# Kernel tuning notes

Hardware: AMD Instinct MI355X
Metric: run time of the kernel (lower is better)

The kernel has to match this reference:

```python
import jax, jax.numpy as jnp
import numpy as np

DIM = 1024
N_EXPERTS = 8
TOP_K = 2
EXPERT_HIDDEN = DIM * 2
B, T = 4, 4096


def setup_inputs() -> dict:
    key = jax.random.key(0)
    ks = jax.random.split(key, 5)
    # xavier_uniform with gain=0.02 for w1/w2 (fan_in=DIM, fan_out=EXPERT_HIDDEN)
    lim12 = 0.02 * np.sqrt(6.0 / (DIM + EXPERT_HIDDEN))
    lim3 = 0.02 * np.sqrt(6.0 / (EXPERT_HIDDEN + DIM))
    x = jax.random.normal(ks[0], (B, T, DIM), dtype=jnp.float32)
    router_w = 0.02 * jax.random.normal(ks[1], (N_EXPERTS, DIM), dtype=jnp.float32)
    w1 = jax.random.uniform(ks[2], (N_EXPERTS, DIM, EXPERT_HIDDEN), minval=-lim12, maxval=lim12, dtype=jnp.float32)
    w2 = jax.random.uniform(ks[3], (N_EXPERTS, DIM, EXPERT_HIDDEN), minval=-lim12, maxval=lim12, dtype=jnp.float32)
    w3 = jax.random.uniform(ks[4], (N_EXPERTS, EXPERT_HIDDEN, DIM), minval=-lim3, maxval=lim3, dtype=jnp.float32)
    return {"x": x, "router_w": router_w, "w1": w1, "w2": w2, "w3": w3}


def reference(x, router_w, w1, w2, w3):
    # Router: top-k softmax gating, renormalized over the selected k.
    logits = jnp.einsum('btd,ed->bte', x, router_w)          # [B,T,E]
    probs = jax.nn.softmax(logits, axis=-1)
    topk_vals, topk_idx = jax.lax.top_k(probs, TOP_K)        # [B,T,K]
    topk_weights = topk_vals / topk_vals.sum(axis=-1, keepdims=True)

    out = jnp.zeros_like(x)
    for e in range(N_EXPERTS):
        # gate weight for expert e per token (0 if e not in token's top-k)
        w_e = jnp.where(topk_idx == e, topk_weights, 0.0).sum(axis=-1)  # [B,T]
        h = jax.nn.silu(jnp.einsum('btd,dh->bth', x, w1[e])) * jnp.einsum('btd,dh->bth', x, w2[e])
        out = out + jnp.einsum('bth,hd->btd', h, w3[e]) * w_e[..., None]
    aux_loss = jnp.float32(0.0)  # eval mode
    return (out, aux_loss)
```

## Files before the change

### kernel.cpp

```cpp
#include <hip/hip_runtime.h>
#include <stdint.h>

#define TTOK 16384
#define NDIM 1024
#define NHID 2048
#define NEXP 8
#define TM 256
#define MAXT 136
#define SLOTCAP (2 * TTOK + NEXP * TM)

typedef __attribute__((ext_vector_type(8))) short short8;
typedef __attribute__((ext_vector_type(4))) float f32x4;

__device__ __forceinline__ unsigned short f2bf(float f) {
  unsigned int u = __float_as_uint(f);
  u += 0x7FFFu + ((u >> 16) & 1u);
  return (unsigned short)(u >> 16);
}

__device__ __forceinline__ void gload16(const void* g, void* l) {
  __builtin_amdgcn_global_load_lds(
      (const __attribute__((address_space(1))) unsigned int*)g,
      (__attribute__((address_space(3))) unsigned int*)l, 16, 0, 0);
}

__device__ __forceinline__ float silu(float z) {
  return z / (1.0f + __expf(-z));
}

__device__ __forceinline__ void router_block(int b, const float* __restrict__ x,
                                             const float* __restrict__ rw,
                                             unsigned short* __restrict__ xbf,
                                             int* __restrict__ tok_e,
                                             float* __restrict__ tok_gw) {
  int t = (b << 2) + (threadIdx.x >> 6);
  int lane = threadIdx.x & 63;
  const float4* xr = (const float4*)(x + (size_t)t * NDIM);

  float4 v[4];
  float d[NEXP];
#pragma unroll
  for (int e = 0; e < NEXP; ++e) d[e] = 0.f;

#pragma unroll
  for (int i = 0; i < 4; ++i) {
    int c = i * 64 + lane;
    v[i] = xr[c];
#pragma unroll
    for (int e = 0; e < NEXP; ++e) {
      float4 w = ((const float4*)(rw + e * NDIM))[c];
      d[e] += v[i].x * w.x + v[i].y * w.y + v[i].z * w.z + v[i].w * w.w;
    }
  }
#pragma unroll
  for (int e = 0; e < NEXP; ++e)
    for (int s = 32; s; s >>= 1) d[e] += __shfl_xor(d[e], s, 64);

  unsigned short* xo = xbf + (size_t)t * NDIM;
#pragma unroll
  for (int i = 0; i < 4; ++i) {
    int c = i * 64 + lane;
    ushort4 u;
    u.x = f2bf(v[i].x); u.y = f2bf(v[i].y); u.z = f2bf(v[i].z); u.w = f2bf(v[i].w);
    ((ushort4*)xo)[c] = u;
  }

  if (lane == 0) {
    float m = d[0];
#pragma unroll
    for (int e = 1; e < NEXP; ++e) m = fmaxf(m, d[e]);
    float ex[NEXP];
#pragma unroll
    for (int e = 0; e < NEXP; ++e) ex[e] = __expf(d[e] - m);
    int e0 = 0;
#pragma unroll
    for (int e = 1; e < NEXP; ++e) if (ex[e] > ex[e0]) e0 = e;
    int e1 = (e0 == 0) ? 1 : 0;
#pragma unroll
    for (int e = 0; e < NEXP; ++e) if (e != e0 && ex[e] > ex[e1]) e1 = e;
    float p0 = ex[e0], p1 = ex[e1];
    float inv = 1.f / (p0 + p1);
    tok_e[2 * t] = e0; tok_e[2 * t + 1] = e1;
    tok_gw[2 * t] = p0 * inv; tok_gw[2 * t + 1] = p1 * inv;
  }
}

__device__ __forceinline__ void tconv_tile(const float* __restrict__ src,
                                           unsigned short* __restrict__ dst,
                                           int R, int C, int bx, int by) {
  __shared__ unsigned short tile[64][65];
  int tx = threadIdx.x & 15, ty = threadIdx.x >> 4;
#pragma unroll
  for (int rr = 0; rr < 4; ++rr) {
    int rl = rr * 16 + ty;
    float4 v = *(const float4*)(src + (size_t)(by + rl) * C + bx + tx * 4);
    tile[rl][tx * 4 + 0] = f2bf(v.x);
    tile[rl][tx * 4 + 1] = f2bf(v.y);
    tile[rl][tx * 4 + 2] = f2bf(v.z);
    tile[rl][tx * 4 + 3] = f2bf(v.w);
  }
  __syncthreads();
#pragma unroll
  for (int rr = 0; rr < 4; ++rr) {
    int cl = rr * 16 + ty;
    ushort4 u;
    u.x = tile[tx * 4 + 0][cl];
    u.y = tile[tx * 4 + 1][cl];
    u.z = tile[tx * 4 + 2][cl];
    u.w = tile[tx * 4 + 3][cl];
    *(ushort4*)(dst + (size_t)(bx + cl) * R + by + tx * 4) = u;
  }
}

__global__ void k_prep(const float* __restrict__ x, const float* __restrict__ rw,
                       unsigned short* __restrict__ xbf, int* __restrict__ tok_e,
                       float* __restrict__ tok_gw, const float* __restrict__ w1,
                       const float* __restrict__ w2, const float* __restrict__ w3,
                       unsigned short* __restrict__ w1t, unsigned short* __restrict__ w2t,
                       unsigned short* __restrict__ w3t) {
  int b = blockIdx.x;
  if (b < 4096) {
    router_block(b, x, rw, xbf, tok_e, tok_gw);
    return;
  }
  int tcb = b - 4096;
  int bx = tcb & 31;
  int by = (tcb >> 5) & 15;
  int z = tcb >> 9;
  if (z < 16) {
    int e = z & 7;
    const float* src = (z < 8 ? w1 : w2) + (size_t)e * NDIM * NHID;
    unsigned short* dst = (z < 8 ? w1t : w2t) + (size_t)e * NDIM * NHID;
    tconv_tile(src, dst, NDIM, NHID, bx * 64, by * 64);
  } else {
    int e = z - 16;
    const float* src = w3 + (size_t)e * NHID * NDIM;
    unsigned short* dst = w3t + (size_t)e * NHID * NDIM;
    tconv_tile(src, dst, NHID, NDIM, by * 64, bx * 64);
  }
}

__global__ void k_count(const int* __restrict__ tok_e, unsigned int* __restrict__ counts) {
  __shared__ unsigned int h[NEXP];
  int tid = threadIdx.x;
  if (tid < NEXP) h[tid] = 0u;
  __syncthreads();
  for (int i = blockIdx.x * 256 + tid; i < 2 * TTOK; i += gridDim.x * 256)
    atomicAdd(&h[tok_e[i]], 1u);
  __syncthreads();
  if (tid < NEXP) atomicAdd(&counts[tid], h[tid]);
}

__global__ void k_offsets(const unsigned int* __restrict__ counts,
                          unsigned int* __restrict__ slotbase, unsigned int* __restrict__ cnt2,
                          unsigned int* __restrict__ tile_e, unsigned int* __restrict__ tile_m0) {
  int l = threadIdx.x;
  unsigned int c[NEXP], base[NEXP], tb[NEXP];
  unsigned int b = 0, t = 0;
#pragma unroll
  for (int e = 0; e < NEXP; ++e) {
    c[e] = counts[e];
    base[e] = b; tb[e] = t;
    unsigned int nt = (c[e] + TM - 1) / TM;
    b += nt * TM; t += nt;
  }
  if (l < NEXP) { slotbase[l] = base[l]; cnt2[l] = 0u; }
  for (int idx = l; idx < MAXT; idx += 64) {
    unsigned int te = 0xFFFFFFFFu, tm = 0;
#pragma unroll
    for (int e = 0; e < NEXP; ++e) {
      unsigned int nt = (c[e] + TM - 1) / TM;
      if ((unsigned)idx >= tb[e] && (unsigned)idx < tb[e] + nt) {
        te = (unsigned)e; tm = base[e] + ((unsigned)idx - tb[e]) * TM;
      }
    }
    tile_e[idx] = te; tile_m0[idx] = tm;
  }
}

__global__ void k_fill(const int* __restrict__ tok_e, const float* __restrict__ tok_gw,
                       const unsigned int* __restrict__ slotbase, unsigned int* __restrict__ cnt2,
                       unsigned int* __restrict__ tok_list, float* __restrict__ gate_list) {
  __shared__ unsigned int hcnt[NEXP];
  __shared__ unsigned int hbase[NEXP];
  int tid = threadIdx.x;
  int t = blockIdx.x * 256 + tid;
  if (tid < NEXP) hcnt[tid] = 0u;
  __syncthreads();
  int e0 = tok_e[2 * t], e1 = tok_e[2 * t + 1];
  float g0 = tok_gw[2 * t], g1 = tok_gw[2 * t + 1];
  unsigned int p0 = atomicAdd(&hcnt[e0], 1u);
  unsigned int p1 = atomicAdd(&hcnt[e1], 1u);
  __syncthreads();
  if (tid < NEXP) hbase[tid] = atomicAdd(&cnt2[tid], hcnt[tid]);
  __syncthreads();
  unsigned int s0 = slotbase[e0] + hbase[e0] + p0;
  unsigned int s1 = slotbase[e1] + hbase[e1] + p1;
  tok_list[s0] = (unsigned)t; gate_list[s0] = g0;
  tok_list[s1] = (unsigned)t; gate_list[s1] = g1;
}

__global__ void k_sentinel(float* __restrict__ out, float v) {
  if (threadIdx.x == 0 && blockIdx.x == 0) out[0] = v;
}

__global__ __launch_bounds__(512, 2) void k_gemm12(
    const unsigned short* __restrict__ xbf, const unsigned short* __restrict__ w1t,
    const unsigned short* __restrict__ w2t, unsigned short* __restrict__ H,
    const unsigned int* __restrict__ tok_list, const unsigned int* __restrict__ tile_e,
    const unsigned int* __restrict__ tile_m0) {
  unsigned int e = tile_e[blockIdx.y];
  if (e > 7u) return;
  int m0 = (int)tile_m0[blockIdx.y];
  int n0 = blockIdx.x * 128;

  __shared__ unsigned short As[2][256 * 64];
  __shared__ unsigned short B1s[2][128 * 64];
  __shared__ unsigned short B2s[2][128 * 64];

  int tid = threadIdx.x, w = tid >> 6, l = tid & 63;
  int rsub = tid >> 3;
  int swb = ((tid & 7) * 16) ^ ((rsub & 7) << 4);

  const unsigned short* aS[4];
#pragma unroll
  for (int jj = 0; jj < 4; ++jj) {
    int row = jj * 64 + rsub;
    aS[jj] = xbf + (size_t)tok_list[m0 + row] * NDIM + (swb >> 1);
  }
  const unsigned short* b1S[2];
  const unsigned short* b2S[2];
#pragma unroll
  for (int jj = 0; jj < 2; ++jj) {
    int row = jj * 64 + rsub;
    size_t off = ((size_t)e * NHID + n0 + row) * NDIM + (swb >> 1);
    b1S[jj] = w1t + off;
    b2S[jj] = w2t + off;
  }
  int ldsb = w * 1024;

  f32x4 acc1[8][2], acc2[8][2];
#pragma unroll
  for (int m = 0; m < 8; ++m)
#pragma unroll
    for (int n = 0; n < 2; ++n) { acc1[m][n] = (f32x4)0.f; acc2[m][n] = (f32x4)0.f; }

  int wr = (w >> 2) * 128, wc = (w & 3) * 32;

  short8 ar[8], b1r[4], b2r[4];

  auto rdA_mh0_B1 = [&](const char* A, const char* B1) {
#pragma unroll
    for (int ks = 0; ks < 2; ++ks) {
      int kb = ks * 64 + ((l >> 4) << 4);
#pragma unroll
      for (int m = 0; m < 4; ++m) {
        int r = wr + m * 16 + (l & 15);
        ar[ks * 4 + m] = *(const short8*)(A + r * 128 + (kb ^ ((r & 7) << 4)));
      }
#pragma unroll
      for (int n = 0; n < 2; ++n) {
        int r = wc + n * 16 + (l & 15);
        b1r[ks * 2 + n] = *(const short8*)(B1 + r * 128 + (kb ^ ((r & 7) << 4)));
      }
    }
  };
  auto rdB2 = [&](const char* B2) {
#pragma unroll
    for (int ks = 0; ks < 2; ++ks) {
      int kb = ks * 64 + ((l >> 4) << 4);
#pragma unroll
      for (int n = 0; n < 2; ++n) {
        int r = wc + n * 16 + (l & 15);
        b2r[ks * 2 + n] = *(const short8*)(B2 + r * 128 + (kb ^ ((r & 7) << 4)));
      }
    }
  };
  auto rdA_mh1 = [&](const char* A) {
#pragma unroll
    for (int ks = 0; ks < 2; ++ks) {
      int kb = ks * 64 + ((l >> 4) << 4);
#pragma unroll
      for (int m = 0; m < 4; ++m) {
        int r = wr + 64 + m * 16 + (l & 15);
        ar[ks * 4 + m] = *(const short8*)(A + r * 128 + (kb ^ ((r & 7) << 4)));
      }
    }
  };
  auto mfma1 = [&](int mh) {
    __builtin_amdgcn_s_setprio(1);
#pragma unroll
    for (int ks = 0; ks < 2; ++ks)
#pragma unroll
      for (int m = 0; m < 4; ++m)
#pragma unroll
        for (int n = 0; n < 2; ++n)
          acc1[mh * 4 + m][n] = __builtin_amdgcn_mfma_f32_16x16x32_bf16(
              ar[ks * 4 + m], b1r[ks * 2 + n], acc1[mh * 4 + m][n], 0, 0, 0);
    __builtin_amdgcn_s_setprio(0);
  };
  auto mfma2 = [&](int mh) {
    __builtin_amdgcn_s_setprio(1);
#pragma unroll
    for (int ks = 0; ks < 2; ++ks)
#pragma unroll
      for (int m = 0; m < 4; ++m)
#pragma unroll
        for (int n = 0; n < 2; ++n)
          acc2[mh * 4 + m][n] = __builtin_amdgcn_mfma_f32_16x16x32_bf16(
              ar[ks * 4 + m], b2r[ks * 2 + n], acc2[mh * 4 + m][n], 0, 0, 0);
    __builtin_amdgcn_s_setprio(0);
  };

  gload16(aS[0], (char*)As[0] + 0 * 8192 + ldsb);
  gload16(aS[2], (char*)As[0] + 2 * 8192 + ldsb);
  gload16(b1S[0], (char*)B1s[0] + 0 * 8192 + ldsb);
  gload16(b1S[1], (char*)B1s[0] + 1 * 8192 + ldsb);
  gload16(aS[1], (char*)As[0] + 1 * 8192 + ldsb);
  gload16(aS[3], (char*)As[0] + 3 * 8192 + ldsb);
  gload16(b2S[0], (char*)B2s[0] + 0 * 8192 + ldsb);
  gload16(b2S[1], (char*)B2s[0] + 1 * 8192 + ldsb);

  for (int t = 0; t < 15; ++t) {
    int cur = t & 1, nxt = cur ^ 1;
    int keN = (t + 1) * 64;
    const char* A = (const char*)As[cur];
    const char* B1 = (const char*)B1s[cur];
    const char* B2 = (const char*)B2s[cur];
    char* An = (char*)As[nxt];
    char* B1n = (char*)B1s[nxt];
    char* B2n = (char*)B2s[nxt];

    gload16(aS[0] + keN, An + 0 * 8192 + ldsb);
    gload16(aS[2] + keN, An + 2 * 8192 + ldsb);
    asm volatile("s_waitcnt vmcnt(6)" ::: "memory");
    __builtin_amdgcn_s_barrier();
    rdA_mh0_B1(A, B1);
    mfma1(0);
    gload16(b1S[0] + keN, B1n + 0 * 8192 + ldsb);
    gload16(b1S[1] + keN, B1n + 1 * 8192 + ldsb);
    asm volatile("s_waitcnt vmcnt(4)" ::: "memory");
    __builtin_amdgcn_s_barrier();
    rdB2(B2);
    mfma2(0);
    gload16(aS[1] + keN, An + 1 * 8192 + ldsb);
    gload16(aS[3] + keN, An + 3 * 8192 + ldsb);
    asm volatile("s_waitcnt vmcnt(6)" ::: "memory");
    __builtin_amdgcn_s_barrier();
    rdA_mh1(A);
    mfma1(1);
    gload16(b2S[0] + keN, B2n + 0 * 8192 + ldsb);
    gload16(b2S[1] + keN, B2n + 1 * 8192 + ldsb);
    __builtin_amdgcn_s_barrier();
    mfma2(1);
  }

  {
    const char* A = (const char*)As[1];
    const char* B1 = (const char*)B1s[1];
    const char* B2 = (const char*)B2s[1];
    asm volatile("s_waitcnt vmcnt(4)" ::: "memory");
    __builtin_amdgcn_s_barrier();
    rdA_mh0_B1(A, B1);
    mfma1(0);
    asm volatile("s_waitcnt vmcnt(0)" ::: "memory");
    __builtin_amdgcn_s_barrier();
    rdB2(B2);
    mfma2(0);
    __builtin_amdgcn_s_barrier();
    rdA_mh1(A);
    mfma1(1);
    __builtin_amdgcn_s_barrier();
    mfma2(1);
  }

#pragma unroll
  for (int m = 0; m < 8; ++m)
#pragma unroll
    for (int n = 0; n < 2; ++n) {
      int col = n0 + wc + n * 16 + (l & 15);
#pragma unroll
      for (int q = 0; q < 4; ++q) {
        int slot = m0 + wr + m * 16 + ((l >> 4) << 2) + q;
        float hv = silu(acc1[m][n][q]) * acc2[m][n][q];
        H[(size_t)slot * NHID + col] = f2bf(hv);
      }
    }
}

__global__ __launch_bounds__(256, 2) void k_gemm3(
    const unsigned short* __restrict__ H, const unsigned short* __restrict__ w3t,
    float* __restrict__ out, const unsigned int* __restrict__ tok_list,
    const float* __restrict__ gate_list, const unsigned int* __restrict__ tile_e,
    const unsigned int* __restrict__ tile_m0) {
  unsigned int e = tile_e[blockIdx.y >> 1];
  if (e > 7u) return;
  int m0 = (int)tile_m0[blockIdx.y >> 1] + (int)(blockIdx.y & 1) * 128;
  int n0 = blockIdx.x * 128;

  __shared__ unsigned short As[128 * 64];
  __shared__ unsigned short Bs[128 * 64];

  int tid = threadIdx.x, w = tid >> 6, l = tid & 63;
  int rsub = tid >> 3;
  int swb = ((tid & 7) * 16) ^ ((rsub & 7) << 4);

  const unsigned short* aS[4];
  const unsigned short* bS[4];
#pragma unroll
  for (int jj = 0; jj < 4; ++jj) {
    int row = jj * 32 + rsub;
    aS[jj] = H + (size_t)(m0 + row) * NHID + (swb >> 1);
    bS[jj] = w3t + ((size_t)e * NDIM + n0 + row) * NHID + (swb >> 1);
  }
  int ldsb = w * 1024;

  f32x4 acc[4][4];
#pragma unroll
  for (int m = 0; m < 4; ++m)
#pragma unroll
    for (int n = 0; n < 4; ++n) acc[m][n] = (f32x4)0.f;

  int wr = (w >> 1) * 64, wc = (w & 1) * 64;

  for (int t = 0; t < 32; ++t) {
    int ke = t * 64;
#pragma unroll
    for (int jj = 0; jj < 4; ++jj) {
      gload16(aS[jj] + ke, (char*)As + jj * 4096 + ldsb);
      gload16(bS[jj] + ke, (char*)Bs + jj * 4096 + ldsb);
    }
    __syncthreads();
#pragma unroll
    for (int ks = 0; ks < 2; ++ks) {
      int kb = ks * 64 + ((l >> 4) << 4);
      short8 a[4], b[4];
#pragma unroll
      for (int m = 0; m < 4; ++m) {
        int r = wr + m * 16 + (l & 15);
        a[m] = *(const short8*)((const char*)As + r * 128 + (kb ^ ((r & 7) << 4)));
      }
#pragma unroll
      for (int n = 0; n < 4; ++n) {
        int r = wc + n * 16 + (l & 15);
        b[n] = *(const short8*)((const char*)Bs + r * 128 + (kb ^ ((r & 7) << 4)));
      }
#pragma unroll
      for (int m = 0; m < 4; ++m)
#pragma unroll
        for (int n = 0; n < 4; ++n)
          acc[m][n] = __builtin_amdgcn_mfma_f32_16x16x32_bf16(a[m], b[n], acc[m][n], 0, 0, 0);
    }
    __syncthreads();
  }

#pragma unroll
  for (int m = 0; m < 4; ++m)
#pragma unroll
    for (int q = 0; q < 4; ++q) {
      int slot = m0 + wr + m * 16 + ((l >> 4) << 2) + q;
      unsigned int tok = tok_list[slot];
      float g = gate_list[slot];
      if (g != 0.f) {
        float* orow = out + (size_t)tok * NDIM + n0 + wc;
#pragma unroll
        for (int n = 0; n < 4; ++n)
          atomicAdd(orow + n * 16 + (l & 15), acc[m][n][q] * g);
      }
    }
}

extern "C" void kernel_launch(void* const* d_in, const int* in_sizes, int n_in,
                              void* d_out, int out_size, void* d_ws, size_t ws_size,
                              hipStream_t stream) {
  const float* x = (const float*)d_in[0];
  const float* rw = (const float*)d_in[1];
  const float* w1 = (const float*)d_in[2];
  const float* w2 = (const float*)d_in[3];
  const float* w3 = (const float*)d_in[4];
  float* out = (float*)d_out;
  char* ws = (char*)d_ws;

  size_t o = 0;
  auto alloc = [&](size_t b) { size_t r = o; o = (o + b + 255) & ~(size_t)255; return r; };
  size_t o_xbf = alloc((size_t)TTOK * NDIM * 2);
  size_t o_w3t = alloc((size_t)NEXP * NDIM * NHID * 2);
  size_t o_H = alloc((size_t)SLOTCAP * NHID * 2);
  size_t o_tok = alloc((size_t)SLOTCAP * 4);
  size_t o_gate = alloc((size_t)SLOTCAP * 4);
  size_t o_te = alloc((size_t)TTOK * 2 * 4);
  size_t o_tg = alloc((size_t)TTOK * 2 * 4);
  size_t o_cnt = alloc(64);
  size_t o_cnt2 = alloc(64);
  size_t o_sb = alloc(64);
  size_t o_tle = alloc(MAXT * 4 + 64);
  size_t o_tlm = alloc(MAXT * 4 + 64);
  size_t need = o;

  size_t outBytes = (size_t)out_size * sizeof(float);
  size_t wtBytes = (size_t)NEXP * NDIM * NHID * 2;

  if (ws_size < need || outBytes < 2 * wtBytes) {
    hipMemsetAsync(d_out, 0, outBytes, stream);
    k_sentinel<<<1, 64, 0, stream>>>(out, (float)((double)ws_size / 1048576.0));
    return;
  }

  unsigned short* xbf = (unsigned short*)(ws + o_xbf);
  unsigned short* w3t = (unsigned short*)(ws + o_w3t);
  unsigned short* Hbuf = (unsigned short*)(ws + o_H);
  unsigned int* tok_list = (unsigned int*)(ws + o_tok);
  float* gate_list = (float*)(ws + o_gate);
  int* tok_e = (int*)(ws + o_te);
  float* tok_gw = (float*)(ws + o_tg);
  unsigned int* counts = (unsigned int*)(ws + o_cnt);
  unsigned int* cnt2 = (unsigned int*)(ws + o_cnt2);
  unsigned int* slotbase = (unsigned int*)(ws + o_sb);
  unsigned int* tile_e = (unsigned int*)(ws + o_tle);
  unsigned int* tile_m0 = (unsigned int*)(ws + o_tlm);

  unsigned short* w1t = (unsigned short*)d_out;
  unsigned short* w2t = (unsigned short*)((char*)d_out + wtBytes);

  hipMemsetAsync(counts, 0, 64, stream);
  hipMemsetAsync(tok_list, 0, (size_t)SLOTCAP * 4, stream);
  hipMemsetAsync(gate_list, 0, (size_t)SLOTCAP * 4, stream);

  k_prep<<<16384, 256, 0, stream>>>(x, rw, xbf, tok_e, tok_gw, w1, w2, w3, w1t, w2t, w3t);
  k_count<<<64, 256, 0, stream>>>(tok_e, counts);
  k_offsets<<<1, 64, 0, stream>>>(counts, slotbase, cnt2, tile_e, tile_m0);
  k_fill<<<TTOK / 256, 256, 0, stream>>>(tok_e, tok_gw, slotbase, cnt2, tok_list, gate_list);

  k_gemm12<<<dim3(NHID / 128, MAXT), 512, 0, stream>>>(xbf, w1t, w2t, Hbuf, tok_list,
                                                       tile_e, tile_m0);

  hipMemsetAsync(d_out, 0, outBytes, stream);

  k_gemm3<<<dim3(NDIM / 128, 2 * MAXT), 256, 0, stream>>>(Hbuf, w3t, out, tok_list, gate_list,
                                                          tile_e, tile_m0);
}
```

Baseline: 690.8 us.

## Replace double-buffered gate/up GEMM pipeline with single-buffered synchronous loop

Shrinks the gate/up GEMM kernel's shared-memory tiles from two buffers to one and drops the interleaved prefetch schedule. Each k-step now issues all global-to-LDS loads, waits for them to finish, computes, then hits a barrier. This halves LDS use, which could allow more resident blocks, but global load latency is no longer hidden behind MFMA work.

Result: slower. 720.0 us (+4.2%).

```diff
diff --git a/kernel.cpp b/kernel.cpp
--- a/kernel.cpp
+++ b/kernel.cpp
@@ -214,9 +214,9 @@
   int m0 = (int)tile_m0[blockIdx.y];
   int n0 = blockIdx.x * 128;
 
-  __shared__ unsigned short As[2][256 * 64];
-  __shared__ unsigned short B1s[2][128 * 64];
-  __shared__ unsigned short B2s[2][128 * 64];
+  __shared__ unsigned short As[256 * 64];
+  __shared__ unsigned short B1s[128 * 64];
+  __shared__ unsigned short B2s[128 * 64];
 
   int tid = threadIdx.x, w = tid >> 6, l = tid & 63;
   int rsub = tid >> 3;
@@ -249,41 +249,41 @@
 
   short8 ar[8], b1r[4], b2r[4];
 
-  auto rdA_mh0_B1 = [&](const char* A, const char* B1) {
+  auto rdA_mh0_B1 = [&]() {
 #pragma unroll
     for (int ks = 0; ks < 2; ++ks) {
       int kb = ks * 64 + ((l >> 4) << 4);
 #pragma unroll
       for (int m = 0; m < 4; ++m) {
         int r = wr + m * 16 + (l & 15);
-        ar[ks * 4 + m] = *(const short8*)(A + r * 128 + (kb ^ ((r & 7) << 4)));
+        ar[ks * 4 + m] = *(const short8*)((const char*)As + r * 128 + (kb ^ ((r & 7) << 4)));
       }
 #pragma unroll
       for (int n = 0; n < 2; ++n) {
         int r = wc + n * 16 + (l & 15);
-        b1r[ks * 2 + n] = *(const short8*)(B1 + r * 128 + (kb ^ ((r & 7) << 4)));
+        b1r[ks * 2 + n] = *(const short8*)((const char*)B1s + r * 128 + (kb ^ ((r & 7) << 4)));
       }
     }
   };
-  auto rdB2 = [&](const char* B2) {
+  auto rdB2 = [&]() {
 #pragma unroll
     for (int ks = 0; ks < 2; ++ks) {
       int kb = ks * 64 + ((l >> 4) << 4);
 #pragma unroll
       for (int n = 0; n < 2; ++n) {
         int r = wc + n * 16 + (l & 15);
-        b2r[ks * 2 + n] = *(const short8*)(B2 + r * 128 + (kb ^ ((r & 7) << 4)));
+        b2r[ks * 2 + n] = *(const short8*)((const char*)B2s + r * 128 + (kb ^ ((r & 7) << 4)));
       }
     }
   };
-  auto rdA_mh1 = [&](const char* A) {
+  auto rdA_mh1 = [&]() {
 #pragma unroll
     for (int ks = 0; ks < 2; ++ks) {
       int kb = ks * 64 + ((l >> 4) << 4);
 #pragma unroll
       for (int m = 0; m < 4; ++m) {
         int r = wr + 64 + m * 16 + (l & 15);
-        ar[ks * 4 + m] = *(const short8*)(A + r * 128 + (kb ^ ((r & 7) << 4)));
+        ar[ks * 4 + m] = *(const short8*)((const char*)As + r * 128 + (kb ^ ((r & 7) << 4)));
       }
     }
   };
@@ -312,66 +312,28 @@
     __builtin_amdgcn_s_setprio(0);
   };
 
-  gload16(aS[0], (char*)As[0] + 0 * 8192 + ldsb);
-  gload16(aS[2], (char*)As[0] + 2 * 8192 + ldsb);
-  gload16(b1S[0], (char*)B1s[0] + 0 * 8192 + ldsb);
-  gload16(b1S[1], (char*)B1s[0] + 1 * 8192 + ldsb);
-  gload16(aS[1], (char*)As[0] + 1 * 8192 + ldsb);
-  gload16(aS[3], (char*)As[0] + 3 * 8192 + ldsb);
-  gload16(b2S[0], (char*)B2s[0] + 0 * 8192 + ldsb);
-  gload16(b2S[1], (char*)B2s[0] + 1 * 8192 + ldsb);
-
-  for (int t = 0; t < 15; ++t) {
-    int cur = t & 1, nxt = cur ^ 1;
-    int keN = (t + 1) * 64;
-    const char* A = (const char*)As[cur];
-    const char* B1 = (const char*)B1s[cur];
-    const char* B2 = (const char*)B2s[cur];
-    char* An = (char*)As[nxt];
-    char* B1n = (char*)B1s[nxt];
-    char* B2n = (char*)B2s[nxt];
-
-    gload16(aS[0] + keN, An + 0 * 8192 + ldsb);
-    gload16(aS[2] + keN, An + 2 * 8192 + ldsb);
-    asm volatile("s_waitcnt vmcnt(6)" ::: "memory");
-    __builtin_amdgcn_s_barrier();
-    rdA_mh0_B1(A, B1);
-    mfma1(0);
-    gload16(b1S[0] + keN, B1n + 0 * 8192 + ldsb);
-    gload16(b1S[1] + keN, B1n + 1 * 8192 + ldsb);
-    asm volatile("s_waitcnt vmcnt(4)" ::: "memory");
-    __builtin_amdgcn_s_barrier();
-    rdB2(B2);
-    mfma2(0);
-    gload16(aS[1] + keN, An + 1 * 8192 + ldsb);
-    gload16(aS[3] + keN, An + 3 * 8192 + ldsb);
-    asm volatile("s_waitcnt vmcnt(6)" ::: "memory");
-    __builtin_amdgcn_s_barrier();
-    rdA_mh1(A);
-    mfma1(1);
-    gload16(b2S[0] + keN, B2n + 0 * 8192 + ldsb);
-    gload16(b2S[1] + keN, B2n + 1 * 8192 + ldsb);
-    __builtin_amdgcn_s_barrier();
-    mfma2(1);
-  }
-
-  {
-    const char* A = (const char*)As[1];
-    const char* B1 = (const char*)B1s[1];
-    const char* B2 = (const char*)B2s[1];
-    asm volatile("s_waitcnt vmcnt(4)" ::: "memory");
-    __builtin_amdgcn_s_barrier();
-    rdA_mh0_B1(A, B1);
-    mfma1(0);
+  for (int t = 0; t < 16; ++t) {
+    int ke = t * 64;
+#pragma unroll
+    for (int jj = 0; jj < 4; ++jj)
+      gload16(aS[jj] + ke, (char*)As + jj * 8192 + ldsb);
+#pragma unroll
+    for (int jj = 0; jj < 2; ++jj) {
+      gload16(b1S[jj] + ke, (char*)B1s + jj * 8192 + ldsb);
+      gload16(b2S[jj] + ke, (char*)B2s + jj * 8192 + ldsb);
+    }
     asm volatile("s_waitcnt vmcnt(0)" ::: "memory");
     __builtin_amdgcn_s_barrier();
-    rdB2(B2);
+
+    rdA_mh0_B1();
+    mfma1(0);
+    rdB2();
     mfma2(0);
+    rdA_mh1();
+    mfma1(1);
+    mfma2(1);
+
     __builtin_amdgcn_s_barrier();
-    rdA_mh1(A);
-    mfma1(1);
-    __builtin_amdgcn_s_barrier();
-    mfma2(1);
   }
 
 #pragma unroll
```
